# Kernel optimization log

Measured on AMD Instinct MI355X. Metric: run time of the kernel, lower is better.

## Reference

```python
import jax, jax.numpy as jnp
import numpy as np

B, F, R, P, C = 2048, 64, 32, 16, 128  # batch, nfeature(dsym), nrole, npattern, dcontext
TAU = 2.0  # posn_attender sharpness


def setup_inputs() -> dict:
    key = jax.random.key(0)
    ks = jax.random.split(key, 16)
    w = lambda k, shape, s=0.05: jax.random.normal(k, shape, jnp.float32) * s
    z = lambda shape: jnp.zeros(shape, jnp.float32)
    return {
        "form": jax.random.normal(ks[0], (B, F, R), jnp.float32),
        "context": jax.random.normal(ks[1], (B, C), jnp.float32),
        "mod_W": w(ks[2], (C, P * 6)), "mod_b": z((P * 6,)),
        "wch_W": w(ks[3], (C, P * F)), "wch_b": z((P * F,)),
        "wdl_W": w(ks[4], (C, P)), "wdl_b": z((P,)),
        "wep_W": w(ks[5], (C, P * 4)), "wep_b": z((P * 4,)),
        "vch_W": w(ks[6], (C, P * F)), "vch_b": z((P * F,)),
        "vep_W": w(ks[7], (C, P * F * 4)), "vep_b": z((P * F * 4,)),
        "wnc_W": w(ks[8], (C, F)), "wnc_b": z((F,)),
        "wnd_W": w(ks[9], (C, 1)), "wnd_b": z((1,)),
        "wne_W": w(ks[10], (C, 1)), "wne_b": z((1,)),
        "m_W": w(ks[11], (3, C, P * F)), "m_Wb": z((3, P * F)),
        "mb_W": w(ks[12], (3, C, P)), "mb_b": z((3, P)),
    }


def _forward(form, context, mod_W, mod_b, wch_W, wch_b, wdl_W, wdl_b,
             wep_W, wep_b, vch_W, vch_b, vep_W, vep_b,
             wnc_W, wnc_b, wnd_W, wnd_b, wne_W, wne_b,
             m_W, m_Wb, mb_W, mb_b):
    nb = form.shape[0]
    lin = lambda W, b: context @ W + b

    # context-conditioned rule weights
    mod = jax.nn.softmax(lin(mod_W, mod_b).reshape(nb, P, 6), axis=-1)
    w_chng = mod[..., 0:1] * lin(wch_W, wch_b).reshape(nb, P, F)
    w_deln = mod[..., 1:2] * lin(wdl_W, wdl_b).reshape(nb, P, 1)
    w_epen = mod[..., 2:] * lin(wep_W, wep_b).reshape(nb, P, 4)
    v_chng = lin(vch_W, vch_b).reshape(nb, P, F)
    v_epen = lin(vep_W, vep_b).reshape(nb, P, F, 4)
    w_nochng = jnp.exp(lin(wnc_W, wnc_b))   # (B, F)
    w_nodeln = jnp.exp(lin(wnd_W, wnd_b))   # (B, 1)
    w_noepen = jnp.exp(lin(wne_W, wne_b))   # (B, 1)

    # Matcher3: trigram (prev, cur, next) feature matching; log-prob summed then exp'd
    prev = jnp.pad(form[:, :, :-1], ((0, 0), (0, 0), (1, 0)))
    nxt = jnp.pad(form[:, :, 1:], ((0, 0), (0, 0), (0, 1)))
    forms3 = jnp.stack([prev, form, nxt], 0)                                   # (3,B,F,R)
    Wk = (jnp.einsum('bc,kcn->kbn', context, m_W) + m_Wb[:, None, :]).reshape(3, nb, P, F)
    bk = jnp.einsum('bc,kcp->kbp', context, mb_W) + mb_b[:, None, :]
    score = jnp.einsum('kbpf,kbfr->kbpr', Wk, forms3) + bk[..., None]
    match = jnp.exp(jnp.sum(jax.nn.log_sigmoid(score), axis=0))                # (B,P,R)

    positions = jnp.arange(R, dtype=form.dtype)

    def posn_attn(posn):  # (B,1) soft position -> (B,R) radial-basis attention
        return jax.nn.softmax(-TAU * (posn - positions[None, :]) ** 2, axis=-1)

    def bind(out, x, attn):  # soft write symbol x at attended role
        a = attn[:, None, :]
        return out * (1.0 - a) + x[:, :, None] * a

    def epen(out, posn, match_i, we_p, ve_p):
        we = match_i * we_p                                                    # (B,P)
        p = jax.nn.sigmoid(jnp.sum(we, 1, keepdims=True) - w_noepen)           # (B,1)
        v = jnp.sum(jax.nn.relu(we)[..., None] * ve_p, 1)                      # (B,F)
        out_ = bind(out, v, posn_attn(posn))
        out = p[..., None] * out_ + (1.0 - p[..., None]) * out
        return out, posn + p

    def step(carry, x):
        out, posn = carry
        sym_i, match_i = x  # (B,F), (B,P)
        # epenthesis before
        out, posn = epen(out, posn, match_i, w_epen[..., 0], v_epen[..., 0])
        # feature change + deletion
        wc = match_i[..., None] * w_chng                                       # (B,P,F)
        p_chng = jax.nn.sigmoid(jnp.sum(wc, 1) - w_nochng)                     # (B,F)
        vc = jnp.sum(jax.nn.relu(wc) * v_chng, 1)                              # (B,F)
        sym = sym_i + p_chng * (vc - sym_i)
        out_ = bind(out, sym, posn_attn(posn))
        wd = match_i[..., None] * w_deln                                       # (B,P,1)
        p_deln = jax.nn.sigmoid(jnp.sum(wd, 1) - w_nodeln)                     # (B,1)
        out = (1.0 - p_deln[..., None]) * out_ + p_deln[..., None] * out
        posn = posn + (1.0 - p_deln)
        # epenthesis after
        out, posn = epen(out, posn, match_i, w_epen[..., 2], v_epen[..., 2])
        return (out, posn), None

    carry0 = (jnp.zeros((nb, F, R), form.dtype), jnp.zeros((nb, 1), form.dtype))
    xs = (jnp.moveaxis(form, 2, 0), jnp.moveaxis(match, 2, 0))
    (out, _), _ = jax.lax.scan(step, carry0, xs)
    return out


def reference(form, context, mod_W, mod_b, wch_W, wch_b, wdl_W, wdl_b,
              wep_W, wep_b, vch_W, vch_b, vep_W, vep_b,
              wnc_W, wnc_b, wnd_W, wnd_b, wne_W, wne_b,
              m_W, m_Wb, mb_W, mb_b):
    return _forward(form, context, mod_W, mod_b, wch_W, wch_b, wdl_W, wdl_b,
                    wep_W, wep_b, vch_W, vch_b, vep_W, vep_b,
                    wnc_W, wnc_b, wnd_W, wnd_b, wne_W, wne_b,
                    m_W, m_Wb, mb_W, mb_b)
```

## Files before the change

### kernel.cpp

```cpp
#include <hip/hip_runtime.h>

#define B_ 2048
#define NTOT 7426
#define YSTRIDE 7432
#define WSTRIDE 8192

typedef unsigned short u16;
typedef unsigned int   u32;
typedef __attribute__((ext_vector_type(2))) float v2f;

__device__ __forceinline__ float bfu(u16 u) {
    u32 i = ((u32)u) << 16; float f; __builtin_memcpy(&f, &i, 4); return f;
}
__device__ __forceinline__ float bflo(u32 w) {
    u32 i = w << 16; float f; __builtin_memcpy(&f, &i, 4); return f;
}
__device__ __forceinline__ float bfhi(u32 w) {
    u32 i = w & 0xffff0000u; float f; __builtin_memcpy(&f, &i, 4); return f;
}
__device__ __forceinline__ u16 f2bf(float v) {
    u32 iv; __builtin_memcpy(&iv, &v, 4);
    u32 r = (iv + 0x7fffu + ((iv >> 16) & 1u)) >> 16;
    return (u16)r;
}
__device__ __forceinline__ float sigm(float x) { return 1.f / (1.f + __expf(-x)); }
__device__ __forceinline__ float lsg(float x) {
    return fminf(x, 0.f) - log1pf(__expf(-fabsf(x)));
}

template<bool F32> __device__ __forceinline__ float LD(const void* p, int e) {
    if (F32) return ((const float*)p)[e];
    return bfu(((const u16*)p)[e]);
}
template<bool F32> __device__ __forceinline__ float2 LD2(const void* p, int e) {
    if (F32) { const float* q = (const float*)p; return make_float2(q[e], q[e + 1]); }
    u32 w = ((const u32*)p)[e >> 1];
    return make_float2(bflo(w), bfhi(w));
}
template<bool F32> __device__ __forceinline__ float4 LD4(const void* p, int e) {
    if (F32) return ((const float4*)p)[e >> 2];
    uint2 w = ((const uint2*)p)[e >> 2];
    return make_float4(bflo(w.x), bfhi(w.x), bflo(w.y), bfhi(w.y));
}
template<bool F32> __device__ __forceinline__ void ST(void* p, int e, float v) {
    if (F32) ((float*)p)[e] = v; else ((u16*)p)[e] = f2bf(v);
}

struct Args {
    const void *form, *ctx;
    const void *mod_W, *mod_b, *wch_W, *wch_b, *wdl_W, *wdl_b, *wep_W, *wep_b;
    const void *vch_W, *vch_b, *vep_W, *vep_b;
    const void *wnc_W, *wnc_b, *wnd_W, *wnd_b, *wne_W, *wne_b;
    const void *m_W, *m_Wb, *mb_W, *mb_b;
    void* outp;
};

__device__ __forceinline__ int probe_is_f32(const void* ctx, int t, int* flag_s) {
    if (t == 0) {
        int sane = 0;
        const u16* q = (const u16*)ctx;
        for (int i = 0; i < 64; ++i) {
            u16 u = q[2 * i];
            int ex = (u >> 7) & 0xFF;
            sane += (u == 0 || (ex >= 112 && ex <= 143)) ? 1 : 0;
        }
        *flag_s = (sane < 32) ? 1 : 0;
    }
    __syncthreads();
    return *flag_s;
}


template<bool F32>
__device__ void repack_body(int idx, const Args& A, float* Wcat, float* bcat) {
    int n = idx & (WSTRIDE - 1);
    int c = idx >> 13;
    float w = 0.f, bb = 0.f;
    if (n < 96)        { w = LD<F32>(A.mod_W, c * 96 + n);   bb = LD<F32>(A.mod_b, n); }
    else if (n < 1120) { int j = n - 96;   w = LD<F32>(A.wch_W, c * 1024 + j); bb = LD<F32>(A.wch_b, j); }
    else if (n < 2144) { int j = n - 1120; w = LD<F32>(A.vch_W, c * 1024 + j); bb = LD<F32>(A.vch_b, j); }
    else if (n < 4192) { int i = n - 2144; int col = 4 * (i >> 1) + 2 * (i & 1);
                         w = LD<F32>(A.vep_W, c * 4096 + col); bb = LD<F32>(A.vep_b, col); }
    else if (n < 7264) { int i = n - 4192; int k = i >> 10, j = i & 1023;
                         w = LD<F32>(A.m_W, (k * 128 + c) * 1024 + j); bb = LD<F32>(A.m_Wb, k * 1024 + j); }
    else if (n < 7312) { int i = n - 7264; int k = i >> 4, p = i & 15;
                         w = LD<F32>(A.mb_W, (k * 128 + c) * 16 + p); bb = LD<F32>(A.mb_b, k * 16 + p); }
    else if (n < 7344) { int i = n - 7312; int col = 4 * (i >> 1) + 2 * (i & 1);
                         w = LD<F32>(A.wep_W, c * 64 + col); bb = LD<F32>(A.wep_b, col); }
    else if (n < 7360) { int j = n - 7344; w = LD<F32>(A.wdl_W, c * 16 + j); bb = LD<F32>(A.wdl_b, j); }
    else if (n < 7424) { int j = n - 7360; w = LD<F32>(A.wnc_W, c * 64 + j); bb = LD<F32>(A.wnc_b, j); }
    else if (n == 7424){ w = LD<F32>(A.wnd_W, c); bb = LD<F32>(A.wnd_b, 0); }
    else if (n == 7425){ w = LD<F32>(A.wne_W, c); bb = LD<F32>(A.wne_b, 0); }
    Wcat[idx] = w;
    if (c == 0) bcat[n] = bb;
}

__global__ __launch_bounds__(256) void repack_kernel(Args A, float* Wcat, float* bcat) {
    __shared__ int dt_s;
    const int t = threadIdx.x;
    int isf32 = probe_is_f32(A.ctx, t, &dt_s);
    int idx = blockIdx.x * 256 + t;
    if (isf32) repack_body<true>(idx, A, Wcat, bcat);
    else       repack_body<false>(idx, A, Wcat, bcat);
}

template<bool F32>
__device__ void gemm3_body(int t, int blk, const void* __restrict__ ctx,
                           const float* __restrict__ Wcat, const float* __restrict__ bcat,
                           float* __restrict__ Y) {
    const int cb = blk & 7;
    const int mb = (blk >> 3) * 16;
    const int n0 = cb * 1024 + 4 * t;
    const float4* W4 = (const float4*)Wcat;
    const int wcol = n0 >> 2;

    float4 bv = *(const float4*)(bcat + n0);
    v2f acc[16][2];
    #pragma unroll
    for (int m = 0; m < 16; ++m) {
        acc[m][0].x = bv.x; acc[m][0].y = bv.y;
        acc[m][1].x = bv.z; acc[m][1].y = bv.w;
    }

    float4 w[4];
    #pragma unroll
    for (int j = 0; j < 4; ++j) w[j] = W4[(size_t)j * 2048 + wcol];

    #pragma unroll 1
    for (int c4 = 0; c4 < 128; c4 += 4) {
        float4 wn[4];
        if (c4 + 4 < 128) {
            #pragma unroll
            for (int j = 0; j < 4; ++j) wn[j] = W4[(size_t)(c4 + 4 + j) * 2048 + wcol];
        }
        #pragma unroll
        for (int m = 0; m < 16; ++m) {
            float4 cv = LD4<F32>(ctx, (mb + m) * 128 + c4);
            float cs[4] = {cv.x, cv.y, cv.z, cv.w};
            #pragma unroll
            for (int j = 0; j < 4; ++j) {
                v2f cc; cc.x = cs[j]; cc.y = cs[j];
                v2f w01; w01.x = w[j].x; w01.y = w[j].y;
                v2f w23; w23.x = w[j].z; w23.y = w[j].w;
                acc[m][0] += cc * w01;
                acc[m][1] += cc * w23;
            }
        }
        #pragma unroll
        for (int j = 0; j < 4; ++j) w[j] = wn[j];
    }

    if (n0 < YSTRIDE) {
        #pragma unroll
        for (int m = 0; m < 16; ++m) {
            float4 s;
            s.x = acc[m][0].x; s.y = acc[m][0].y; s.z = acc[m][1].x; s.w = acc[m][1].y;
            *(float4*)(Y + (size_t)(mb + m) * YSTRIDE + n0) = s;
        }
    }
}

__global__ __launch_bounds__(256, 4) void gemm3_kernel(Args A, const float* Wcat,
                                                       const float* bcat, float* Y) {
    __shared__ int dt_s;
    const int t = threadIdx.x, blk = blockIdx.x;
    int isf32 = probe_is_f32(A.ctx, t, &dt_s);
    if (isf32) gemm3_body<true>(t, blk, A.ctx, Wcat, bcat, Y);
    else       gemm3_body<false>(t, blk, A.ctx, Wcat, bcat, Y);
}

struct PD { const void* p0; int off; int st; int mode; float b0, b1; };

template<bool F32>
__device__ __forceinline__ void resolve(const Args& A, int n0, PD& d) {
    if (n0 < 96) {
        d.mode = 0; d.p0 = A.mod_W; d.off = n0; d.st = 96;
        float2 b = LD2<F32>(A.mod_b, n0); d.b0 = b.x; d.b1 = b.y;
    } else if (n0 < 1120) {
        int j = n0 - 96;
        d.mode = 0; d.p0 = A.wch_W; d.off = j; d.st = 1024;
        float2 b = LD2<F32>(A.wch_b, j); d.b0 = b.x; d.b1 = b.y;
    } else if (n0 < 2144) {
        int j = n0 - 1120;
        d.mode = 0; d.p0 = A.vch_W; d.off = j; d.st = 1024;
        float2 b = LD2<F32>(A.vch_b, j); d.b0 = b.x; d.b1 = b.y;
    } else if (n0 < 4192) {
        int u = (n0 - 2144) >> 1;
        d.mode = 1; d.p0 = A.vep_W; d.off = 4 * u; d.st = 4096;
        float4 b = LD4<F32>(A.vep_b, 4 * u); d.b0 = b.x; d.b1 = b.z;
    } else if (n0 < 7264) {
        int i = n0 - 4192; int k = i >> 10, j = i & 1023;
        d.mode = 0; d.p0 = A.m_W; d.off = k * 131072 + j; d.st = 1024;
        float2 b = LD2<F32>(A.m_Wb, k * 1024 + j); d.b0 = b.x; d.b1 = b.y;
    } else if (n0 < 7312) {
        int i = n0 - 7264; int k = i >> 4, p = i & 15;
        d.mode = 0; d.p0 = A.mb_W; d.off = k * 2048 + p; d.st = 16;
        float2 b = LD2<F32>(A.mb_b, k * 16 + p); d.b0 = b.x; d.b1 = b.y;
    } else if (n0 < 7344) {
        int u = (n0 - 7312) >> 1;
        d.mode = 1; d.p0 = A.wep_W; d.off = 4 * u; d.st = 64;
        float4 b = LD4<F32>(A.wep_b, 4 * u); d.b0 = b.x; d.b1 = b.z;
    } else if (n0 < 7360) {
        int j = n0 - 7344;
        d.mode = 0; d.p0 = A.wdl_W; d.off = j; d.st = 16;
        float2 b = LD2<F32>(A.wdl_b, j); d.b0 = b.x; d.b1 = b.y;
    } else if (n0 < 7424) {
        int j = n0 - 7360;
        d.mode = 0; d.p0 = A.wnc_W; d.off = j; d.st = 64;
        float2 b = LD2<F32>(A.wnc_b, j); d.b0 = b.x; d.b1 = b.y;
    } else if (n0 == 7424) {
        d.mode = 2; d.p0 = A.wnd_W; d.off = 0; d.st = 1;
        d.b0 = LD<F32>(A.wnd_b, 0); d.b1 = LD<F32>(A.wne_b, 0);
    } else {
        d.mode = 3; d.p0 = A.mod_W; d.off = 0; d.st = 0; d.b0 = 0.f; d.b1 = 0.f;
    }
}

template<bool F32>
__device__ __forceinline__ v2f fetchw(const PD& d, const Args& A, int c) {
    if (d.mode == 0) {
        float2 w = LD2<F32>(d.p0, d.off + c * d.st);
        v2f r; r.x = w.x; r.y = w.y; return r;
    } else if (d.mode == 1) {
        float4 q = LD4<F32>(d.p0, d.off + c * d.st);
        v2f r; r.x = q.x; r.y = q.z; return r;
    } else if (d.mode == 2) {
        v2f r; r.x = LD<F32>(A.wnd_W, c); r.y = LD<F32>(A.wne_W, c); return r;
    }
    v2f r; r.x = 0.f; r.y = 0.f; return r;
}

template<bool F32>
__device__ void gemm_body(float (*ctx_s)[128], int t, int blk, const Args& A, float* Y) {
    const int cb = blk & 3;
    const int mb = (blk >> 2) * 8;
    {
        int m = t >> 5, c0 = (t & 31) * 4;
        float4 v = LD4<F32>(A.ctx, (mb + m) * 128 + c0);
        ctx_s[m][c0] = v.x; ctx_s[m][c0 + 1] = v.y; ctx_s[m][c0 + 2] = v.z; ctx_s[m][c0 + 3] = v.w;
    }
    __syncthreads();
    PD d[4]; int n0[4];
    #pragma unroll
    for (int i = 0; i < 4; ++i) { n0[i] = cb * 2048 + i * 512 + 2 * t; resolve<F32>(A, n0[i], d[i]); }
    v2f acc[4][8];
    #pragma unroll
    for (int i = 0; i < 4; ++i)
        #pragma unroll
        for (int m = 0; m < 8; ++m) { acc[i][m].x = d[i].b0; acc[i][m].y = d[i].b1; }
    for (int c4 = 0; c4 < 32; ++c4) {
        float cv[8][4];
        #pragma unroll
        for (int m = 0; m < 8; ++m) *(float4*)cv[m] = *(const float4*)&ctx_s[m][c4 * 4];
        #pragma unroll
        for (int j = 0; j < 4; ++j) {
            int c = c4 * 4 + j;
            v2f w[4];
            #pragma unroll
            for (int i = 0; i < 4; ++i) w[i] = fetchw<F32>(d[i], A, c);
            #pragma unroll
            for (int m = 0; m < 8; ++m) {
                v2f cvv; cvv.x = cv[m][j]; cvv.y = cv[m][j];
                #pragma unroll
                for (int i = 0; i < 4; ++i) acc[i][m] += cvv * w[i];
            }
        }
    }
    #pragma unroll
    for (int i = 0; i < 4; ++i) {
        if (d[i].mode < 3) {
            #pragma unroll
            for (int m = 0; m < 8; ++m) {
                float2 s; s.x = acc[i][m].x; s.y = acc[i][m].y;
                *(float2*)(Y + (size_t)(mb + m) * YSTRIDE + n0[i]) = s;
            }
        }
    }
}

__global__ __launch_bounds__(256) void gemm_kernel(Args A, float* Y) {
    __shared__ float ctx_s[8][128];
    __shared__ int dt_s;
    const int t = threadIdx.x, blk = blockIdx.x;
    int isf32 = probe_is_f32(A.ctx, t, &dt_s);
    if (isf32) gemm_body<true>(ctx_s, t, blk, A, Y);
    else       gemm_body<false>(ctx_s, t, blk, A, Y);
}

struct __align__(16) ScanSmem {
    float U[6144];
    float V[3072];
    float form_s[64 * 33];
    float match_s[512];
    float wnc_s[64];
    float wep0_s[16], wep2_s[16], wdl_s[16];
    float coef_s[96];
    float sc_s[2];
};

template<bool F32>
__device__ void scan_body(ScanSmem& S, int t, int b, const Args& A, const float* __restrict__ Y) {
    float* Wk_s = S.U;
    float* bk_s = S.U + 3072;
    float* modl = S.U + 3120;
    float* xtab = S.U;
    float* wch_s = S.V;
    float* vch_s = S.V + 1024;
    float* rlI   = S.V + 2048;
    float* gtab  = S.V;

    const float* Yr = Y + (size_t)b * YSTRIDE;
    const float4* Y4 = (const float4*)Yr;

    const int f_own = t & 63;
    const int fq    = t >> 6;

    const float2* vep2p = (const float2*)(Yr + 2144);
    v2f vepf[16];
    #pragma unroll
    for (int p = 0; p < 16; ++p) {
        float2 v = vep2p[p * 64 + f_own];
        vepf[p].x = v.x; vepf[p].y = v.y;
    }

    {
        int e0 = b * 2048 + t * 8;
        float4 x = LD4<F32>(A.form, e0);
        float4 y = LD4<F32>(A.form, e0 + 4);
        int f = t >> 2, r0 = (t & 3) * 8;
        float* dst = S.form_s + f * 33 + r0;
        dst[0] = x.x; dst[1] = x.y; dst[2] = x.z; dst[3] = x.w;
        dst[4] = y.x; dst[5] = y.y; dst[6] = y.z; dst[7] = y.w;
    }
    for (int i = t; i < 768; i += 256) ((float4*)Wk_s)[i] = Y4[1048 + i];
    if (t < 12) ((float4*)bk_s)[t] = Y4[1816 + t];
    if (t < 24) ((float4*)modl)[t] = Y4[t];
    ((float4*)wch_s)[t] = Y4[24 + t];
    ((float4*)vch_s)[t] = Y4[280 + t];
    if (t < 16) {
        S.wep0_s[t] = Yr[7312 + 2 * t];
        S.wep2_s[t] = Yr[7312 + 2 * t + 1];
        S.wdl_s[t]  = Yr[7344 + t];
    } else if (t >= 32 && t < 96) {
        S.wnc_s[t - 32] = __expf(Yr[7360 + (t - 32)]);
    } else if (t >= 96 && t < 98) {
        S.sc_s[t - 96] = __expf(Yr[7424 + (t - 96)]);
    }
    __syncthreads();

    if (t < 16) {
        float v[6]; float mx = -1e30f;
        #pragma unroll
        for (int j = 0; j < 6; ++j) { v[j] = modl[t * 6 + j]; mx = fmaxf(mx, v[j]); }
        float s = 0.f;
        #pragma unroll
        for (int j = 0; j < 6; ++j) { v[j] = __expf(v[j] - mx); s += v[j]; }
        float inv = 1.f / s;
        #pragma unroll
        for (int j = 0; j < 6; ++j) modl[t * 6 + j] = v[j] * inv;
    }
    __syncthreads();

    if (t < 16) {
        S.wep0_s[t] *= modl[t * 6 + 2];
        S.wep2_s[t] *= modl[t * 6 + 4];
        S.wdl_s[t]  *= modl[t * 6 + 1];
    }
    for (int i = t; i < 1024; i += 256) wch_s[i] *= modl[(i >> 6) * 6];

    const int my_r = t & 31;
    #pragma unroll 1
    for (int it = 0; it < 2; ++it) {
        int idx = t + 256 * it;
        int p = idx >> 5, r = idx & 31;
        float s0 = bk_s[p], s1 = bk_s[16 + p], s2 = bk_s[32 + p];
        const float4* w0 = (const float4*)(Wk_s + p * 64);
        const float4* w1 = (const float4*)(Wk_s + (16 + p) * 64);
        const float4* w2 = (const float4*)(Wk_s + (32 + p) * 64);
        for (int f4 = 0; f4 < 16; ++f4) {
            float a0[4], a1[4], a2[4];
            *(float4*)a0 = w0[f4]; *(float4*)a1 = w1[f4]; *(float4*)a2 = w2[f4];
            #pragma unroll
            for (int j = 0; j < 4; ++j) {
                int f = f4 * 4 + j;
                float f0 = S.form_s[f * 33 + r];
                float fm = __shfl_up(f0, 1, 32);   if (r == 0)  fm = 0.f;
                float fp = __shfl_down(f0, 1, 32); if (r == 31) fp = 0.f;
                s0 += a0[j] * fm; s1 += a1[j] * f0; s2 += a2[j] * fp;
            }
        }
        S.match_s[p * 32 + r] = __expf(lsg(s0) + lsg(s1) + lsg(s2));
    }
    __syncthreads();

    if (t < 96) {
        int sub = t >> 5, r = t & 31;
        const float* w = (sub == 0) ? S.wep0_s : (sub == 1) ? S.wdl_s : S.wep2_s;
        float s = 0.f;
        for (int p = 0; p < 16; ++p) s += S.match_s[p * 32 + r] * w[p];
        float cf;
        if (sub == 1) cf = 1.f - sigm(s - S.sc_s[0]);
        else          cf = sigm(s - S.sc_s[1]);
        S.coef_s[sub * 32 + r] = cf;
    }
    for (int i = t; i < 512; i += 256) {
        int p = i >> 5, r = i & 31;
        float m = S.match_s[p * 32 + r];
        rlI[2 * i]     = fmaxf(m * S.wep0_s[p], 0.f);
        rlI[2 * i + 1] = fmaxf(m * S.wep2_s[p], 0.f);
    }
    float wchf[16], vchf[16];
    #pragma unroll
    for (int p = 0; p < 16; ++p) {
        wchf[p] = wch_s[p * 64 + f_own];
        vchf[p] = vch_s[p * 64 + f_own];
    }
    const float wncf = S.wnc_s[f_own];
    __syncthreads();

    #pragma unroll 1
    for (int j = 0; j < 8; ++j) {
        int rs = fq * 8 + j;
        v2f v02; v02.x = 0.f; v02.y = 0.f;
        float sum = 0.f, vs1 = 0.f;
        const v2f* rlp = (const v2f*)(rlI + 2 * rs);
        #pragma unroll
        for (int p = 0; p < 16; ++p) {
            v2f rl = rlp[p * 32];
            v02 += rl * vepf[p];
            float m = S.match_s[p * 32 + rs];
            float wc = m * wchf[p];
            sum += wc;
            vs1 += fmaxf(wc, 0.f) * vchf[p];
        }
        float pch = sigm(sum - wncf);
        float si  = S.form_s[f_own * 33 + rs];
        xtab[0 * 2048 + rs * 64 + f_own] = v02.x;
        xtab[1 * 2048 + rs * 64 + f_own] = si + pch * (vs1 - si);
        xtab[2 * 2048 + rs * 64 + f_own] = v02.y;
    }
    __syncthreads();

    float* ck_s  = S.match_s;
    float* pos_s = S.match_s + 128;
    if (t < 96) ck_s[t] = S.coef_s[(t % 3) * 32 + (t / 3)];
    __syncthreads();
    if (t < 64) {
        float a = ck_s[t];
        float a0 = a;
        #pragma unroll
        for (int d = 1; d < 64; d <<= 1) { float v = __shfl_up(a, d, 64); if (t >= d) a += v; }
        pos_s[t] = a - a0;
        float carry = __shfl(a, 63, 64);
        float b2 = (t < 32) ? ck_s[64 + t] : 0.f;
        float c2 = b2;
        #pragma unroll
        for (int d = 1; d < 32; d <<= 1) { float v = __shfl_up(c2, d, 32); if ((t & 31) >= d) c2 += v; }
        if (t < 32) pos_s[64 + t] = carry + c2 - b2;
    }
    __syncthreads();

    #pragma unroll 1
    for (int i = 0; i < 12; ++i) {
        int idx = t + 256 * i;
        int k = idx >> 5, r = idx & 31;
        float posn = pos_s[k];
        float pc = fminf(posn, 31.f);
        float ci = floorf(pc + 0.5f);
        float dmin = posn - ci;
        float dd = posn - (float)r;
        float eo = __expf(-2.f * (dd * dd - dmin * dmin));
        float Z = eo;
        Z += __shfl_xor(Z, 1, 32);
        Z += __shfl_xor(Z, 2, 32);
        Z += __shfl_xor(Z, 4, 32);
        Z += __shfl_xor(Z, 8, 32);
        Z += __shfl_xor(Z, 16, 32);
        gtab[idx] = ck_s[k] * eo / Z;
    }
    __syncthreads();

    const int fgrp = t >> 5;
    v2f o01, o23, o45, o67;
    o01 = 0.f; o23 = 0.f; o45 = 0.f; o67 = 0.f;
    #pragma unroll 1
    for (int rs = 0; rs < 32; ++rs) {
        #pragma unroll
        for (int sub = 0; sub < 3; ++sub) {
            float g = gtab[(rs * 3 + sub) * 32 + my_r];
            v2f gv; gv.x = g; gv.y = g;
            const float4* xb = (const float4*)(xtab + sub * 2048 + rs * 64 + fgrp * 8);
            float4 xa = xb[0], xc = xb[1];
            v2f x01, x23, x45, x67;
            x01.x = xa.x; x01.y = xa.y; x23.x = xa.z; x23.y = xa.w;
            x45.x = xc.x; x45.y = xc.y; x67.x = xc.z; x67.y = xc.w;
            o01 += gv * (x01 - o01);
            o23 += gv * (x23 - o23);
            o45 += gv * (x45 - o45);
            o67 += gv * (x67 - o67);
        }
    }

    float oreg[8] = {o01.x, o01.y, o23.x, o23.y, o45.x, o45.y, o67.x, o67.y};
    #pragma unroll
    for (int i = 0; i < 8; ++i) {
        ST<F32>(A.outp, b * 2048 + (fgrp * 8 + i) * 32 + my_r, oreg[i]);
    }
}

__global__ __launch_bounds__(256) void scan_kernel(Args A, const float* Y) {
    __shared__ ScanSmem S;
    __shared__ int dt_s;
    const int t = threadIdx.x, b = blockIdx.x;
    int isf32 = probe_is_f32(A.ctx, t, &dt_s);
    if (isf32) scan_body<true>(S, t, b, A, Y);
    else       scan_body<false>(S, t, b, A, Y);
}

struct Smem {
    float U[6144];
    float form_s[64 * 33];
    float match_s[512];
    float wch_s[1024];
    float vch_s[1024];
    float vep0_s[1024];
    float vep2_s[1024];
    float wep0_s[16], wep2_s[16], wdl_s[16];
    float wnc_s[64];
    float sc_s[2];
    float ssum_s[96];
};

template<bool F32>
__device__ void mono_body(Smem& S, int t, int b, const Args& A) {
    float* c_s  = S.U;
    float* modl = S.U + 128;
    float* Wk_s = S.U + 224;
    float* bk_s = S.U + 3344;
    float* xtab = S.U;

    if (t < 128) c_s[t] = LD<F32>(A.ctx, b * 128 + t);
    {
        int e0 = b * 2048 + t * 8;
        float4 x = LD4<F32>(A.form, e0);
        float4 y = LD4<F32>(A.form, e0 + 4);
        int f = t >> 2, r0 = (t & 3) * 8;
        float* dst = S.form_s + f * 33 + r0;
        dst[0] = x.x; dst[1] = x.y; dst[2] = x.z; dst[3] = x.w;
        dst[4] = y.x; dst[5] = y.y; dst[6] = y.z; dst[7] = y.w;
    }
    __syncthreads();
    if (t < 96) {
        float a = LD<F32>(A.mod_b, t);
        for (int cc = 0; cc < 128; ++cc) a += c_s[cc] * LD<F32>(A.mod_W, cc * 96 + t);
        modl[t] = a;
    }
    __syncthreads();
    if (t < 16) {
        float v[6]; float mx = -1e30f;
        #pragma unroll
        for (int j = 0; j < 6; ++j) { v[j] = modl[t * 6 + j]; mx = fmaxf(mx, v[j]); }
        float s = 0.f;
        #pragma unroll
        for (int j = 0; j < 6; ++j) { v[j] = __expf(v[j] - mx); s += v[j]; }
        float inv = 1.f / s;
        #pragma unroll
        for (int j = 0; j < 6; ++j) modl[t * 6 + j] = v[j] * inv;
    }
    __syncthreads();
    for (int j = t; j < 512; j += 256) {
        int n0 = j * 2;
        float2 bb = LD2<F32>(A.wch_b, n0);
        float a0 = bb.x, a1 = bb.y;
        for (int cc = 0; cc < 128; ++cc) {
            float2 w = LD2<F32>(A.wch_W, cc * 1024 + n0); float cv = c_s[cc];
            a0 += cv * w.x; a1 += cv * w.y;
        }
        int p = n0 >> 6; float sc = modl[p * 6 + 0];
        S.wch_s[n0] = sc * a0; S.wch_s[n0 + 1] = sc * a1;
    }
    for (int j = t; j < 512; j += 256) {
        int n0 = j * 2;
        float2 bb = LD2<F32>(A.vch_b, n0);
        float a0 = bb.x, a1 = bb.y;
        for (int cc = 0; cc < 128; ++cc) {
            float2 w = LD2<F32>(A.vch_W, cc * 1024 + n0); float cv = c_s[cc];
            a0 += cv * w.x; a1 += cv * w.y;
        }
        S.vch_s[n0] = a0; S.vch_s[n0 + 1] = a1;
    }
    for (int u = t; u < 1024; u += 256) {
        int n0 = u * 4;
        float4 bb = LD4<F32>(A.vep_b, n0);
        float a0 = bb.x, a2 = bb.z;
        for (int cc = 0; cc < 128; ++cc) {
            float4 w = LD4<F32>(A.vep_W, cc * 4096 + n0); float cv = c_s[cc];
            a0 += cv * w.x; a2 += cv * w.z;
        }
        S.vep0_s[u] = a0; S.vep2_s[u] = a2;
    }
    for (int j = t; j < 1536; j += 256) {
        int k  = j >> 9;
        int jj = j & 511;
        int n0 = jj * 2;
        float2 bb = LD2<F32>(A.m_Wb, k * 1024 + n0);
        float a0 = bb.x, a1 = bb.y;
        for (int cc = 0; cc < 128; ++cc) {
            float2 w = LD2<F32>(A.m_W, (k * 128 + cc) * 1024 + n0); float cv = c_s[cc];
            a0 += cv * w.x; a1 += cv * w.y;
        }
        int p = n0 >> 6, f = n0 & 63;
        Wk_s[(k * 16 + p) * 65 + f]     = a0;
        Wk_s[(k * 16 + p) * 65 + f + 1] = a1;
    }
    if (t < 16) {
        int n0 = t * 4;
        float4 bb = LD4<F32>(A.wep_b, n0);
        float a0 = bb.x, a2 = bb.z;
        for (int cc = 0; cc < 128; ++cc) {
            float4 w = LD4<F32>(A.wep_W, cc * 64 + n0); float cv = c_s[cc];
            a0 += cv * w.x; a2 += cv * w.z;
        }
        S.wep0_s[t] = modl[t * 6 + 2] * a0;
        S.wep2_s[t] = modl[t * 6 + 4] * a2;
    } else if (t < 32) {
        int p = t - 16;
        float a = LD<F32>(A.wdl_b, p);
        for (int cc = 0; cc < 128; ++cc) a += c_s[cc] * LD<F32>(A.wdl_W, cc * 16 + p);
        S.wdl_s[p] = modl[p * 6 + 1] * a;
    } else if (t < 96) {
        int f = t - 32;
        float a = LD<F32>(A.wnc_b, f);
        for (int cc = 0; cc < 128; ++cc) a += c_s[cc] * LD<F32>(A.wnc_W, cc * 64 + f);
        S.wnc_s[f] = __expf(a);
    } else if (t < 98) {
        const void* W  = (t == 96) ? A.wnd_W : A.wne_W;
        const void* bb = (t == 96) ? A.wnd_b : A.wne_b;
        float a = LD<F32>(bb, 0);
        for (int cc = 0; cc < 128; ++cc) a += c_s[cc] * LD<F32>(W, cc);
        S.sc_s[t - 96] = __expf(a);
    } else if (t < 146) {
        int i = t - 98;
        int k = i >> 4, p = i & 15;
        float a = LD<F32>(A.mb_b, k * 16 + p);
        for (int cc = 0; cc < 128; ++cc) a += c_s[cc] * LD<F32>(A.mb_W, (k * 128 + cc) * 16 + p);
        bk_s[i] = a;
    }
    __syncthreads();
    for (int idx = t; idx < 512; idx += 256) {
        int p = idx >> 5, r = idx & 31;
        float s0 = bk_s[p], s1 = bk_s[16 + p], s2 = bk_s[32 + p];
        const float* w0 = Wk_s + p * 65;
        const float* w1 = Wk_s + (16 + p) * 65;
        const float* w2 = Wk_s + (32 + p) * 65;
        for (int f = 0; f < 64; ++f) {
            const float* fr = S.form_s + f * 33 + r;
            float fm1 = (r > 0)  ? fr[-1] : 0.f;
            float f0  = fr[0];
            float fp1 = (r < 31) ? fr[1]  : 0.f;
            s0 += w0[f] * fm1; s1 += w1[f] * f0; s2 += w2[f] * fp1;
        }
        S.match_s[p * 32 + r] = __expf(lsg(s0) + lsg(s1) + lsg(s2));
    }
    __syncthreads();
    if (t < 96) {
        int which = t >> 5, r = t & 31;
        const float* w = (which == 0) ? S.wep0_s : (which == 1) ? S.wep2_s : S.wdl_s;
        float s = 0.f;
        for (int p = 0; p < 16; ++p) s += S.match_s[p * 32 + r] * w[p];
        S.ssum_s[which * 32 + r] = s;
    }
    #pragma unroll 1
    for (int q = 0; q < 24; ++q) {
        int idx = t + 256 * q;
        int sub = idx >> 11;
        int rs  = (idx >> 6) & 31;
        int f   = idx & 63;
        float x;
        if (sub == 1) {
            float sum = 0.f, vs = 0.f;
            for (int p = 0; p < 16; ++p) {
                float wc = S.match_s[p * 32 + rs] * S.wch_s[p * 64 + f];
                sum += wc;
                vs  += fmaxf(wc, 0.f) * S.vch_s[p * 64 + f];
            }
            float pch = sigm(sum - S.wnc_s[f]);
            float si  = S.form_s[f * 33 + rs];
            x = si + pch * (vs - si);
        } else {
            const float* wep = (sub == 0) ? S.wep0_s : S.wep2_s;
            const float* vep = (sub == 0) ? S.vep0_s : S.vep2_s;
            float vs = 0.f;
            for (int p = 0; p < 16; ++p) {
                float w = S.match_s[p * 32 + rs] * wep[p];
                vs += fmaxf(w, 0.f) * vep[p * 64 + f];
            }
            x = vs;
        }
        xtab[idx] = x;
    }
    __syncthreads();
    const int my_r = t & 31;
    const int fgrp = t >> 5;
    float oreg[8];
    #pragma unroll
    for (int i = 0; i < 8; ++i) oreg[i] = 0.f;
    float posn = 0.f;
    const float wnd1v = S.sc_s[0];
    const float wne1v = S.sc_s[1];
    for (int rs = 0; rs < 32; ++rs) {
        #pragma unroll
        for (int sub = 0; sub < 3; ++sub) {
            float coef;
            if (sub == 1) coef = 1.f - sigm(S.ssum_s[64 + rs] - wnd1v);
            else          coef = sigm(S.ssum_s[(sub & 2) * 16 + rs] - wne1v);
            float pc = fminf(posn, 31.f);
            int ci = (int)(pc + 0.5f);
            int lo = ci - 4; if (lo < 0)  lo = 0;
            int hi = ci + 4; if (hi > 31) hi = 31;
            float dmin = posn - (float)ci;
            float mx = -2.f * dmin * dmin;
            float Z = 0.f, eo = 0.f;
            for (int r = lo; r <= hi; ++r) {
                float d = posn - (float)r;
                float e = __expf(-2.f * d * d - mx);
                Z += e;
                if (r == my_r) eo = e;
            }
            float g = coef * eo / Z;
            const float* xb = xtab + (sub * 2048 + rs * 64 + fgrp * 8);
            #pragma unroll
            for (int i = 0; i < 8; ++i) oreg[i] += g * (xb[i] - oreg[i]);
            posn += coef;
        }
    }
    #pragma unroll
    for (int i = 0; i < 8; ++i) {
        ST<F32>(A.outp, b * 2048 + (fgrp * 8 + i) * 32 + my_r, oreg[i]);
    }
}

__global__ __launch_bounds__(256) void phon_mono(Args A) {
    __shared__ Smem S;
    __shared__ int dt_s;
    const int t = threadIdx.x, b = blockIdx.x;
    int isf32 = probe_is_f32(A.ctx, t, &dt_s);
    if (isf32) mono_body<true>(S, t, b, A);
    else       mono_body<false>(S, t, b, A);
}

extern "C" void kernel_launch(void* const* d_in, const int* in_sizes, int n_in,
                              void* d_out, int out_size, void* d_ws, size_t ws_size,
                              hipStream_t stream) {
    Args A;
    A.form  = d_in[0];  A.ctx   = d_in[1];
    A.mod_W = d_in[2];  A.mod_b = d_in[3];
    A.wch_W = d_in[4];  A.wch_b = d_in[5];
    A.wdl_W = d_in[6];  A.wdl_b = d_in[7];
    A.wep_W = d_in[8];  A.wep_b = d_in[9];
    A.vch_W = d_in[10]; A.vch_b = d_in[11];
    A.vep_W = d_in[12]; A.vep_b = d_in[13];
    A.wnc_W = d_in[14]; A.wnc_b = d_in[15];
    A.wnd_W = d_in[16]; A.wnd_b = d_in[17];
    A.wne_W = d_in[18]; A.wne_b = d_in[19];
    A.m_W   = d_in[20]; A.m_Wb  = d_in[21];
    A.mb_W  = d_in[22]; A.mb_b  = d_in[23];
    A.outp  = d_out;

    const size_t needY = (size_t)B_ * YSTRIDE * sizeof(float);
    const size_t needW = needY + ((size_t)128 * WSTRIDE + WSTRIDE) * sizeof(float);
    if (ws_size >= needW) {
        float* Y    = (float*)d_ws;
        float* Wcat = Y + (size_t)B_ * YSTRIDE;
        float* bcat = Wcat + (size_t)128 * WSTRIDE;
        repack_kernel<<<(128 * WSTRIDE) / 256, 256, 0, stream>>>(A, Wcat, bcat);
        gemm3_kernel<<<1024, 256, 0, stream>>>(A, Wcat, bcat, Y);
        scan_kernel<<<B_, 256, 0, stream>>>(A, Y);
    } else if (ws_size >= needY) {
        float* Y = (float*)d_ws;
        gemm_kernel<<<1024, 256, 0, stream>>>(A, Y);
        scan_kernel<<<B_, 256, 0, stream>>>(A, Y);
    } else {
        phon_mono<<<B_, 256, 0, stream>>>(A);
    }
}
```

Before: 293.6 us.

## Shrink GEMM row tile, stage context in LDS, pair-wise repack, slim scan smem

The GEMM kernel now handles 8 batch rows per block instead of 16 and stages those context rows in shared memory, doubling the grid to 2048 blocks. Accumulator register pressure drops and occupancy can rise, at the cost of re-reading each weight column twice as often. The repack kernel now writes two columns per thread using the existing resolve/fetchw helpers. In the scan kernel the form tile moves into an aliased region of the U buffer and each thread's form values are held in registers, which reduces shared memory use per block.

```diff
diff --git a/kernel.cpp b/kernel.cpp
--- a/kernel.cpp
+++ b/kernel.cpp
@@ -68,105 +68,6 @@
     }
     __syncthreads();
     return *flag_s;
-}
-
-
-template<bool F32>
-__device__ void repack_body(int idx, const Args& A, float* Wcat, float* bcat) {
-    int n = idx & (WSTRIDE - 1);
-    int c = idx >> 13;
-    float w = 0.f, bb = 0.f;
-    if (n < 96)        { w = LD<F32>(A.mod_W, c * 96 + n);   bb = LD<F32>(A.mod_b, n); }
-    else if (n < 1120) { int j = n - 96;   w = LD<F32>(A.wch_W, c * 1024 + j); bb = LD<F32>(A.wch_b, j); }
-    else if (n < 2144) { int j = n - 1120; w = LD<F32>(A.vch_W, c * 1024 + j); bb = LD<F32>(A.vch_b, j); }
-    else if (n < 4192) { int i = n - 2144; int col = 4 * (i >> 1) + 2 * (i & 1);
-                         w = LD<F32>(A.vep_W, c * 4096 + col); bb = LD<F32>(A.vep_b, col); }
-    else if (n < 7264) { int i = n - 4192; int k = i >> 10, j = i & 1023;
-                         w = LD<F32>(A.m_W, (k * 128 + c) * 1024 + j); bb = LD<F32>(A.m_Wb, k * 1024 + j); }
-    else if (n < 7312) { int i = n - 7264; int k = i >> 4, p = i & 15;
-                         w = LD<F32>(A.mb_W, (k * 128 + c) * 16 + p); bb = LD<F32>(A.mb_b, k * 16 + p); }
-    else if (n < 7344) { int i = n - 7312; int col = 4 * (i >> 1) + 2 * (i & 1);
-                         w = LD<F32>(A.wep_W, c * 64 + col); bb = LD<F32>(A.wep_b, col); }
-    else if (n < 7360) { int j = n - 7344; w = LD<F32>(A.wdl_W, c * 16 + j); bb = LD<F32>(A.wdl_b, j); }
-    else if (n < 7424) { int j = n - 7360; w = LD<F32>(A.wnc_W, c * 64 + j); bb = LD<F32>(A.wnc_b, j); }
-    else if (n == 7424){ w = LD<F32>(A.wnd_W, c); bb = LD<F32>(A.wnd_b, 0); }
-    else if (n == 7425){ w = LD<F32>(A.wne_W, c); bb = LD<F32>(A.wne_b, 0); }
-    Wcat[idx] = w;
-    if (c == 0) bcat[n] = bb;
-}
-
-__global__ __launch_bounds__(256) void repack_kernel(Args A, float* Wcat, float* bcat) {
-    __shared__ int dt_s;
-    const int t = threadIdx.x;
-    int isf32 = probe_is_f32(A.ctx, t, &dt_s);
-    int idx = blockIdx.x * 256 + t;
-    if (isf32) repack_body<true>(idx, A, Wcat, bcat);
-    else       repack_body<false>(idx, A, Wcat, bcat);
-}
-
-template<bool F32>
-__device__ void gemm3_body(int t, int blk, const void* __restrict__ ctx,
-                           const float* __restrict__ Wcat, const float* __restrict__ bcat,
-                           float* __restrict__ Y) {
-    const int cb = blk & 7;
-    const int mb = (blk >> 3) * 16;
-    const int n0 = cb * 1024 + 4 * t;
-    const float4* W4 = (const float4*)Wcat;
-    const int wcol = n0 >> 2;
-
-    float4 bv = *(const float4*)(bcat + n0);
-    v2f acc[16][2];
-    #pragma unroll
-    for (int m = 0; m < 16; ++m) {
-        acc[m][0].x = bv.x; acc[m][0].y = bv.y;
-        acc[m][1].x = bv.z; acc[m][1].y = bv.w;
-    }
-
-    float4 w[4];
-    #pragma unroll
-    for (int j = 0; j < 4; ++j) w[j] = W4[(size_t)j * 2048 + wcol];
-
-    #pragma unroll 1
-    for (int c4 = 0; c4 < 128; c4 += 4) {
-        float4 wn[4];
-        if (c4 + 4 < 128) {
-            #pragma unroll
-            for (int j = 0; j < 4; ++j) wn[j] = W4[(size_t)(c4 + 4 + j) * 2048 + wcol];
-        }
-        #pragma unroll
-        for (int m = 0; m < 16; ++m) {
-            float4 cv = LD4<F32>(ctx, (mb + m) * 128 + c4);
-            float cs[4] = {cv.x, cv.y, cv.z, cv.w};
-            #pragma unroll
-            for (int j = 0; j < 4; ++j) {
-                v2f cc; cc.x = cs[j]; cc.y = cs[j];
-                v2f w01; w01.x = w[j].x; w01.y = w[j].y;
-                v2f w23; w23.x = w[j].z; w23.y = w[j].w;
-                acc[m][0] += cc * w01;
-                acc[m][1] += cc * w23;
-            }
-        }
-        #pragma unroll
-        for (int j = 0; j < 4; ++j) w[j] = wn[j];
-    }
-
-    if (n0 < YSTRIDE) {
-        #pragma unroll
-        for (int m = 0; m < 16; ++m) {
-            float4 s;
-            s.x = acc[m][0].x; s.y = acc[m][0].y; s.z = acc[m][1].x; s.w = acc[m][1].y;
-            *(float4*)(Y + (size_t)(mb + m) * YSTRIDE + n0) = s;
-        }
-    }
-}
-
-__global__ __launch_bounds__(256, 4) void gemm3_kernel(Args A, const float* Wcat,
-                                                       const float* bcat, float* Y) {
-    __shared__ int dt_s;
-    const int t = threadIdx.x, blk = blockIdx.x;
-    int isf32 = probe_is_f32(A.ctx, t, &dt_s);
-    if (isf32) gemm3_body<true>(t, blk, A.ctx, Wcat, bcat, Y);
-    else       gemm3_body<false>(t, blk, A.ctx, Wcat, bcat, Y);
 }
 
 struct PD { const void* p0; int off; int st; int mode; float b0, b1; };
@@ -231,6 +132,101 @@
 }
 
 template<bool F32>
+__device__ void repack_body(int pid, const Args& A, float* Wcat, float* bcat) {
+    int n0 = 2 * (pid & 4095);
+    int c  = pid >> 12;
+    PD d;
+    resolve<F32>(A, n0, d);
+    v2f w = fetchw<F32>(d, A, c);
+    float2 s; s.x = w.x; s.y = w.y;
+    *(float2*)(Wcat + (size_t)c * WSTRIDE + n0) = s;
+    if (c == 0) { bcat[n0] = d.b0; bcat[n0 + 1] = d.b1; }
+}
+
+__global__ __launch_bounds__(256) void repack_kernel(Args A, float* Wcat, float* bcat) {
+    __shared__ int dt_s;
+    const int t = threadIdx.x;
+    int isf32 = probe_is_f32(A.ctx, t, &dt_s);
+    int pid = blockIdx.x * 256 + t;
+    if (isf32) repack_body<true>(pid, A, Wcat, bcat);
+    else       repack_body<false>(pid, A, Wcat, bcat);
+}
+
+template<bool F32>
+__device__ void gemm4_body(float* ctx_s, int t, int blk, const void* __restrict__ ctx,
+                           const float* __restrict__ Wcat, const float* __restrict__ bcat,
+                           float* __restrict__ Y) {
+    const int cb = blk & 7;
+    const int mb = (blk >> 3) * 8;
+
+    {
+        int m = t >> 5, c0 = (t & 31) * 4;
+        float4 v = LD4<F32>(ctx, (mb + m) * 128 + c0);
+        *(float4*)&ctx_s[m * 128 + c0] = v;
+    }
+    __syncthreads();
+
+    const int n0 = cb * 1024 + 4 * t;
+    const float4* W4 = (const float4*)Wcat;
+    const int wcol = n0 >> 2;
+
+    float4 bv = *(const float4*)(bcat + n0);
+    v2f acc[8][2];
+    #pragma unroll
+    for (int m = 0; m < 8; ++m) {
+        acc[m][0].x = bv.x; acc[m][0].y = bv.y;
+        acc[m][1].x = bv.z; acc[m][1].y = bv.w;
+    }
+
+    float4 w[4];
+    #pragma unroll
+    for (int j = 0; j < 4; ++j) w[j] = W4[(size_t)j * 2048 + wcol];
+
+    #pragma unroll 1
+    for (int c4 = 0; c4 < 128; c4 += 4) {
+        float4 wn[4];
+        if (c4 + 4 < 128) {
+            #pragma unroll
+            for (int j = 0; j < 4; ++j) wn[j] = W4[(size_t)(c4 + 4 + j) * 2048 + wcol];
+        }
+        #pragma unroll
+        for (int m = 0; m < 8; ++m) {
+            float4 cv = *(const float4*)&ctx_s[m * 128 + c4];
+            float cs[4] = {cv.x, cv.y, cv.z, cv.w};
+            #pragma unroll
+            for (int j = 0; j < 4; ++j) {
+                v2f cc; cc.x = cs[j]; cc.y = cs[j];
+                v2f w01; w01.x = w[j].x; w01.y = w[j].y;
+                v2f w23; w23.x = w[j].z; w23.y = w[j].w;
+                acc[m][0] += cc * w01;
+                acc[m][1] += cc * w23;
+            }
+        }
+        #pragma unroll
+        for (int j = 0; j < 4; ++j) w[j] = wn[j];
+    }
+
+    if (n0 < YSTRIDE) {
+        #pragma unroll
+        for (int m = 0; m < 8; ++m) {
+            float4 s;
+            s.x = acc[m][0].x; s.y = acc[m][0].y; s.z = acc[m][1].x; s.w = acc[m][1].y;
+            *(float4*)(Y + (size_t)(mb + m) * YSTRIDE + n0) = s;
+        }
+    }
+}
+
+__global__ __launch_bounds__(256) void gemm4_kernel(Args A, const float* Wcat,
+                                                    const float* bcat, float* Y) {
+    __shared__ float ctx_s[8 * 128];
+    __shared__ int dt_s;
+    const int t = threadIdx.x, blk = blockIdx.x;
+    int isf32 = probe_is_f32(A.ctx, t, &dt_s);
+    if (isf32) gemm4_body<true>(ctx_s, t, blk, A.ctx, Wcat, bcat, Y);
+    else       gemm4_body<false>(ctx_s, t, blk, A.ctx, Wcat, bcat, Y);
+}
+
+template<bool F32>
 __device__ void gemm_body(float (*ctx_s)[128], int t, int blk, const Args& A, float* Y) {
     const int cb = blk & 3;
     const int mb = (blk >> 2) * 8;
@@ -290,7 +286,6 @@
 struct __align__(16) ScanSmem {
     float U[6144];
     float V[3072];
-    float form_s[64 * 33];
     float match_s[512];
     float wnc_s[64];
     float wep0_s[16], wep2_s[16], wdl_s[16];
@@ -300,14 +295,15 @@
 
 template<bool F32>
 __device__ void scan_body(ScanSmem& S, int t, int b, const Args& A, const float* __restrict__ Y) {
-    float* Wk_s = S.U;
-    float* bk_s = S.U + 3072;
-    float* modl = S.U + 3120;
-    float* xtab = S.U;
-    float* wch_s = S.V;
-    float* vch_s = S.V + 1024;
-    float* rlI   = S.V + 2048;
-    float* gtab  = S.V;
+    float* Wk_s   = S.U;
+    float* bk_s   = S.U + 3072;
+    float* modl   = S.U + 3120;
+    float* form_s = S.U + 3312;
+    float* xtab   = S.U;
+    float* wch_s  = S.V;
+    float* vch_s  = S.V + 1024;
+    float* rlI    = S.V + 2048;
+    float* gtab   = S.V;
 
     const float* Yr = Y + (size_t)b * YSTRIDE;
     const float4* Y4 = (const float4*)Yr;
@@ -328,7 +324,7 @@
         float4 x = LD4<F32>(A.form, e0);
         float4 y = LD4<F32>(A.form, e0 + 4);
         int f = t >> 2, r0 = (t & 3) * 8;
-        float* dst = S.form_s + f * 33 + r0;
+        float* dst = form_s + f * 33 + r0;
         dst[0] = x.x; dst[1] = x.y; dst[2] = x.z; dst[3] = x.w;
         dst[4] = y.x; dst[5] = y.y; dst[6] = y.z; dst[7] = y.w;
     }
@@ -383,7 +379,7 @@
             #pragma unroll
             for (int j = 0; j < 4; ++j) {
                 int f = f4 * 4 + j;
-                float f0 = S.form_s[f * 33 + r];
+                float f0 = form_s[f * 33 + r];
                 float fm = __shfl_up(f0, 1, 32);   if (r == 0)  fm = 0.f;
                 float fp = __shfl_down(f0, 1, 32); if (r == 31) fp = 0.f;
                 s0 += a0[j] * fm; s1 += a1[j] * f0; s2 += a2[j] * fp;
@@ -416,6 +412,9 @@
         vchf[p] = vch_s[p * 64 + f_own];
     }
     const float wncf = S.wnc_s[f_own];
+    float si_r[8];
+    #pragma unroll
+    for (int j = 0; j < 8; ++j) si_r[j] = form_s[f_own * 33 + fq * 8 + j];
     __syncthreads();
 
     #pragma unroll 1
@@ -434,7 +433,7 @@
             vs1 += fmaxf(wc, 0.f) * vchf[p];
         }
         float pch = sigm(sum - wncf);
-        float si  = S.form_s[f_own * 33 + rs];
+        float si  = si_r[j];
         xtab[0 * 2048 + rs * 64 + f_own] = v02.x;
         xtab[1 * 2048 + rs * 64 + f_own] = si + pch * (vs1 - si);
         xtab[2 * 2048 + rs * 64 + f_own] = v02.y;
@@ -773,8 +772,8 @@
         float* Y    = (float*)d_ws;
         float* Wcat = Y + (size_t)B_ * YSTRIDE;
         float* bcat = Wcat + (size_t)128 * WSTRIDE;
-        repack_kernel<<<(128 * WSTRIDE) / 256, 256, 0, stream>>>(A, Wcat, bcat);
-        gemm3_kernel<<<1024, 256, 0, stream>>>(A, Wcat, bcat, Y);
+        repack_kernel<<<(128 * WSTRIDE / 2) / 256, 256, 0, stream>>>(A, Wcat, bcat);
+        gemm4_kernel<<<2048, 256, 0, stream>>>(A, Wcat, bcat, Y);
         scan_kernel<<<B_, 256, 0, stream>>>(A, Y);
     } else if (ws_size >= needY) {
         float* Y = (float*)d_ws;
```

After: 274.1 us. -6.6%, faster.
